# Performance work log

Measured on AMD Instinct MI355X. Metric: run time of the kernel, lower is better.

## Reference

```python
import jax, jax.numpy as jnp
import numpy as np

N_QUBITS = 8    # out_channels = number of wires
KERNEL = 4      # kernel_size
N_LAYERS = 3
PAD = 1
STRIDE = 1


def _gate_rx(t):
    c = jnp.cos(t / 2).astype(jnp.complex64)
    s = (-1j) * jnp.sin(t / 2).astype(jnp.complex64)
    return jnp.stack([jnp.stack([c, s]), jnp.stack([s, c])])


def _gate_ry(t):
    c = jnp.cos(t / 2).astype(jnp.complex64)
    s = jnp.sin(t / 2).astype(jnp.complex64)
    return jnp.stack([jnp.stack([c, -s]), jnp.stack([s, c])])


def _gate_rz(t):
    tc = t.astype(jnp.complex64)
    e0 = jnp.exp(-0.5j * tc)
    e1 = jnp.exp(0.5j * tc)
    z = jnp.zeros_like(e0)
    return jnp.stack([jnp.stack([e0, z]), jnp.stack([z, e1])])


def _apply1(state, gate, q):
    # state: (W, 2, ..., 2); shared 2x2 gate on qubit axis 1+q
    s = jnp.moveaxis(state, 1 + q, -1)
    s = jnp.einsum('...a,ba->...b', s, gate)
    return jnp.moveaxis(s, -1, 1 + q)


def _apply_ry_batched(state, theta, q):
    # per-window RY angles theta: (W,)
    c = jnp.cos(theta / 2)
    s = jnp.sin(theta / 2)
    g = jnp.stack([jnp.stack([c, -s], -1), jnp.stack([s, c], -1)], -2).astype(jnp.complex64)  # (W,2,2)
    st = jnp.moveaxis(state, 1 + q, -1)
    st = jnp.einsum('w...a,wba->w...b', st, g)
    return jnp.moveaxis(st, -1, 1 + q)


def _apply_cnot(state, c, t):
    # control qubit c, target qubit t (axes 1+c, 1+t)
    s = jnp.moveaxis(state, 1 + c, 1)
    ta = 2 + t if t < c else 1 + t
    s = jnp.moveaxis(s, ta, 2)
    s = jnp.stack([s[:, 0], jnp.flip(s[:, 1], axis=1)], axis=1)
    s = jnp.moveaxis(s, 2, ta)
    return jnp.moveaxis(s, 1, 1 + c)


def _ansatz(state, w):
    # custom_ansatz: per wire j: RX(w[j]); CNOT; RY(w[j]); CNOT; RZ(w[j]) with ring entanglement
    for j in range(N_QUBITS):
        cw, tw = (j, j + 1) if j < N_QUBITS - 1 else (0, N_QUBITS - 1)
        state = _apply1(state, _gate_rx(w[j]), j)
        state = _apply_cnot(state, cw, tw)
        state = _apply1(state, _gate_ry(w[j]), j)
        state = _apply_cnot(state, cw, tw)
        state = _apply1(state, _gate_rz(w[j]), j)
    return state

_ansatz_ckpt = jax.checkpoint(_ansatz)


@jax.jit
def _circuit(windows, weights):
    # windows: (W, KERNEL); weights: (N_LAYERS+1, N_QUBITS)
    W = windows.shape[0]
    state = jnp.zeros((W,) + (2,) * N_QUBITS, jnp.complex64)
    state = state.at[(slice(None),) + (0,) * N_QUBITS].set(1.0)
    state = _ansatz_ckpt(state, weights[0])
    for k in range(KERNEL):  # 'no_reupload' data encoding, once
        state = _apply_ry_batched(state, windows[:, k], k)
    for i in range(1, N_LAYERS + 1):
        state = _ansatz_ckpt(state, weights[i])
    probs = state.real ** 2 + state.imag ** 2
    evs = []
    for j in range(N_QUBITS):
        axes = tuple(a for a in range(1, N_QUBITS + 1) if a != 1 + j)
        p = probs.sum(axis=axes)  # (W, 2)
        evs.append(p[:, 0] - p[:, 1])
    return jnp.stack(evs, axis=-1)  # (W, N_QUBITS)


def setup_inputs() -> dict:
    key = jax.random.key(0)
    k1, k2 = jax.random.split(key)
    vector = jax.random.normal(k1, (32, 1, 512), jnp.float32)
    weights = jax.random.uniform(k2, (N_LAYERS + 1, N_QUBITS), jnp.float32, 0.0, 2.0 * np.pi)
    return {"vector": vector, "weights": weights}


def reference(vector, weights):
    bs, ch, l = vector.shape
    if ch > 1:
        vector = vector.mean(axis=1, keepdims=True)
    v = jnp.pad(vector[:, 0], ((0, 0), (PAD, PAD)))
    l_out = (l + 2 * PAD - KERNEL) // STRIDE + 1
    idx = jnp.arange(0, l_out, STRIDE)[:, None] + jnp.arange(KERNEL)[None, :]
    windows = v[:, idx].reshape(-1, KERNEL)  # (bs*l_out, KERNEL)
    out = _circuit(windows, weights)
    return out.reshape(bs, l_out, N_QUBITS).transpose(0, 2, 1).astype(jnp.float32)
```

## Files before the change

### kernel.cpp

```cpp
#include <hip/hip_runtime.h>
#include <math.h>


#define DEV __device__ __forceinline__

#define NQ 8
#define LOUT 511
#define LIN 512
#define BS 32
#define NPAIR 136

DEV float sx(float v, int m) { return __shfl_xor(v, m, 64); }

template<int J>
DEV void rot_rx(float (&re)[4], float (&im)[4], float c, float s) {
    if constexpr (J == 0) {
        float r0=re[0], i0=im[0], r2=re[2], i2=im[2];
        re[0]=c*r0+s*i2; im[0]=c*i0-s*r2; re[2]=c*r2+s*i0; im[2]=c*i2-s*r0;
        float r1=re[1], i1=im[1], r3=re[3], i3=im[3];
        re[1]=c*r1+s*i3; im[1]=c*i1-s*r3; re[3]=c*r3+s*i1; im[3]=c*i3-s*r1;
    } else if constexpr (J == 1) {
        float r0=re[0], i0=im[0], r1=re[1], i1=im[1];
        re[0]=c*r0+s*i1; im[0]=c*i0-s*r1; re[1]=c*r1+s*i0; im[1]=c*i1-s*r0;
        float r2=re[2], i2=im[2], r3=re[3], i3=im[3];
        re[2]=c*r2+s*i3; im[2]=c*i2-s*r3; re[3]=c*r3+s*i2; im[3]=c*i3-s*r2;
    } else {
        constexpr int m = 1 << (7 - J);
        #pragma unroll
        for (int r = 0; r < 4; ++r) {
            float pre = sx(re[r], m), pim = sx(im[r], m);
            re[r] = c*re[r] + s*pim;
            im[r] = c*im[r] - s*pre;
        }
    }
}

template<int J>
DEV void rot_ry(float (&re)[4], float (&im)[4], float c, float s, int lane) {
    if constexpr (J == 0) {
        float r0=re[0], i0=im[0], r2=re[2], i2=im[2];
        re[0]=c*r0-s*r2; im[0]=c*i0-s*i2; re[2]=s*r0+c*r2; im[2]=s*i0+c*i2;
        float r1=re[1], i1=im[1], r3=re[3], i3=im[3];
        re[1]=c*r1-s*r3; im[1]=c*i1-s*i3; re[3]=s*r1+c*r3; im[3]=s*i1+c*i3;
    } else if constexpr (J == 1) {
        float r0=re[0], i0=im[0], r1=re[1], i1=im[1];
        re[0]=c*r0-s*r1; im[0]=c*i0-s*i1; re[1]=s*r0+c*r1; im[1]=s*i0+c*i1;
        float r2=re[2], i2=im[2], r3=re[3], i3=im[3];
        re[2]=c*r2-s*r3; im[2]=c*i2-s*i3; re[3]=s*r2+c*r3; im[3]=s*i2+c*i3;
    } else {
        constexpr int m = 1 << (7 - J);
        float sg = (lane & m) ? s : -s;
        #pragma unroll
        for (int r = 0; r < 4; ++r) {
            float pre = sx(re[r], m), pim = sx(im[r], m);
            re[r] = c*re[r] + sg*pre;
            im[r] = c*im[r] + sg*pim;
        }
    }
}

template<int J>
DEV void rot_rz(float (&re)[4], float (&im)[4], float c, float s, int lane) {
    if constexpr (J == 0) {
        float t;
        t=re[0]; re[0]=c*t+s*im[0]; im[0]=c*im[0]-s*t;
        t=re[1]; re[1]=c*t+s*im[1]; im[1]=c*im[1]-s*t;
        t=re[2]; re[2]=c*t-s*im[2]; im[2]=c*im[2]+s*t;
        t=re[3]; re[3]=c*t-s*im[3]; im[3]=c*im[3]+s*t;
    } else if constexpr (J == 1) {
        float t;
        t=re[0]; re[0]=c*t+s*im[0]; im[0]=c*im[0]-s*t;
        t=re[2]; re[2]=c*t+s*im[2]; im[2]=c*im[2]-s*t;
        t=re[1]; re[1]=c*t-s*im[1]; im[1]=c*im[1]+s*t;
        t=re[3]; re[3]=c*t-s*im[3]; im[3]=c*im[3]+s*t;
    } else {
        constexpr int m = 1 << (7 - J);
        float sg = (lane & m) ? -s : s;
        #pragma unroll
        for (int r = 0; r < 4; ++r) {
            float t = re[r];
            re[r] = c*t + sg*im[r];
            im[r] = c*im[r] - sg*t;
        }
    }
}

template<int J>
DEV void cnot_w(float (&re)[4], float (&im)[4], int lane) {
    if constexpr (J == 0) {
        float t;
        t=re[2]; re[2]=re[3]; re[3]=t;
        t=im[2]; im[2]=im[3]; im[3]=t;
    } else if constexpr (J == 1) {
        re[1]=sx(re[1],32); im[1]=sx(im[1],32);
        re[3]=sx(re[3],32); im[3]=sx(im[3],32);
    } else if constexpr (J == 7) {
        re[2]=sx(re[2],1); im[2]=sx(im[2],1);
        re[3]=sx(re[3],1); im[3]=sx(im[3],1);
    } else {
        constexpr int mc = 1 << (7 - J);
        constexpr int mt = 1 << (6 - J);
        bool ctrl = (lane & mc) != 0;
        #pragma unroll
        for (int r = 0; r < 4; ++r) {
            float pre = sx(re[r], mt), pim = sx(im[r], mt);
            re[r] = ctrl ? pre : re[r];
            im[r] = ctrl ? pim : im[r];
        }
    }
}

template<int J>
DEV void wire(float (&re)[4], float (&im)[4], float ang, int lane) {
    float h = 0.5f * ang;
    float c = __cosf(h);
    float s = __sinf(h);
    rot_rx<J>(re, im, c, s);
    cnot_w<J>(re, im, lane);
    rot_ry<J>(re, im, c, s, lane);
    cnot_w<J>(re, im, lane);
    rot_rz<J>(re, im, c, s, lane);
}

DEV void ansatz(float (&re)[4], float (&im)[4], const float* __restrict__ w, int lane) {
    wire<0>(re, im, w[0], lane);
    wire<1>(re, im, w[1], lane);
    wire<2>(re, im, w[2], lane);
    wire<3>(re, im, w[3], lane);
    wire<4>(re, im, w[4], lane);
    wire<5>(re, im, w[5], lane);
    wire<6>(re, im, w[6], lane);
    wire<7>(re, im, w[7], lane);
}

__global__ __launch_bounds__(64) void kA1(const float* __restrict__ wts,
                                          float2* __restrict__ q) {
    int lane = threadIdx.x;
    int b = blockIdx.x;
    float re[4] = {0.f,0.f,0.f,0.f}, im[4] = {0.f,0.f,0.f,0.f};
    if (lane == 0) re[0] = 1.0f;
    ansatz(re, im, wts, lane);

    if (b & 1) {
        float t;
        t=re[0]; re[0]=-re[2]; re[2]=t;  t=im[0]; im[0]=-im[2]; im[2]=t;
        t=re[1]; re[1]=-re[3]; re[3]=t;  t=im[1]; im[1]=-im[3]; im[3]=t;
    }
    if (b & 2) {
        float t;
        t=re[0]; re[0]=-re[1]; re[1]=t;  t=im[0]; im[0]=-im[1]; im[1]=t;
        t=re[2]; re[2]=-re[3]; re[3]=t;  t=im[2]; im[2]=-im[3]; im[3]=t;
    }
    if (b & 4) {
        bool hi = (lane & 32) != 0;
        #pragma unroll
        for (int r = 0; r < 4; ++r) {
            float pre = sx(re[r],32), pim = sx(im[r],32);
            re[r] = hi ? pre : -pre;
            im[r] = hi ? pim : -pim;
        }
    }
    if (b & 8) {
        bool hi = (lane & 16) != 0;
        #pragma unroll
        for (int r = 0; r < 4; ++r) {
            float pre = sx(re[r],16), pim = sx(im[r],16);
            re[r] = hi ? pre : -pre;
            im[r] = hi ? pim : -pim;
        }
    }
    ansatz(re, im, wts + 8,  lane);
    ansatz(re, im, wts + 16, lane);
    ansatz(re, im, wts + 24, lane);
    #pragma unroll
    for (int r = 0; r < 4; ++r)
        q[b*256 + r*64 + lane] = make_float2(re[r], im[r]);
}

__global__ __launch_bounds__(64) void kA2(const float2* __restrict__ q,
                                          float* __restrict__ Sc) {
    int lane = threadIdx.x;
    int m = blockIdx.x;
    int b = 0, rem = m;
    while (rem >= 16 - b) { rem -= 16 - b; ++b; }
    int bp = b + rem;

    float pp[4];
    #pragma unroll
    for (int rr = 0; rr < 4; ++rr) {
        float2 x = q[b *256 + rr*64 + lane];
        float2 y = q[bp*256 + rr*64 + lane];
        pp[rr] = x.x*y.x + x.y*y.y;
    }
    float a0  = (pp[0]+pp[1]) - (pp[2]+pp[3]);
    float a1  = (pp[0]+pp[2]) - (pp[1]+pp[3]);
    float tot =  pp[0]+pp[1]+pp[2]+pp[3];

    #pragma unroll
    for (int mk = 1; mk <= 32; mk <<= 1) { a0 += sx(a0, mk); a1 += sx(a1, mk); }
    #pragma unroll
    for (int mk = 1; mk <= 32; mk <<= 1) {
        float p = sx(tot, mk);
        tot = (lane & mk) ? (p - tot) : (tot + p);
    }
    float scale = (b == bp) ? 1.0f : 2.0f;
    if (lane == 0) { Sc[m*8+0] = scale*a0; Sc[m*8+1] = scale*a1; }
    if (lane == 32) Sc[m*8+2] = scale*tot;
    if (lane == 16) Sc[m*8+3] = scale*tot;
    if (lane ==  8) Sc[m*8+4] = scale*tot;
    if (lane ==  4) Sc[m*8+5] = scale*tot;
    if (lane ==  2) Sc[m*8+6] = scale*tot;
    if (lane ==  1) Sc[m*8+7] = scale*tot;
}

__global__ __launch_bounds__(64) void kB(const float* __restrict__ vec,
                                         const float* __restrict__ Sc,
                                         float* __restrict__ out) {
    int lane = threadIdx.x;
    int o    = blockIdx.x * 64 + lane;
    int bat  = blockIdx.y;
    bool valid = o < LOUT;
    int oc = valid ? o : 0;

    float cs[4], sn[4];
    #pragma unroll
    for (int k = 0; k < 4; ++k) {
        int p = oc + k;
        float x = (p >= 1 && p <= LIN) ? vec[bat*LIN + p - 1] : 0.f;
        sn[k] = __sinf(0.5f*x);
        cs[k] = __cosf(0.5f*x);
    }
    float t[16];
    #pragma unroll
    for (int i = 0; i < 16; ++i)
        t[i] = ((i&1)?sn[0]:cs[0]) * ((i&2)?sn[1]:cs[1])
             * ((i&4)?sn[2]:cs[2]) * ((i&8)?sn[3]:cs[3]);

    float acc[8] = {0.f,0.f,0.f,0.f,0.f,0.f,0.f,0.f};
    int m = 0;
    #pragma unroll
    for (int b = 0; b < 16; ++b) {
        #pragma unroll
        for (int bp = b; bp < 16; ++bp) {
            float p = t[b] * t[bp];
            #pragma unroll
            for (int j = 0; j < 8; ++j)
                acc[j] = fmaf(Sc[m*8 + j], p, acc[j]);
            ++m;
        }
    }
    if (valid) {
        #pragma unroll
        for (int j = 0; j < 8; ++j)
            out[(bat*NQ + j)*LOUT + o] = acc[j];
    }
}

extern "C" void kernel_launch(void* const* d_in, const int* in_sizes, int n_in,
                              void* d_out, int out_size, void* d_ws, size_t ws_size,
                              hipStream_t stream) {
    const float* vec = (const float*)d_in[0];
    const float* wts = (const float*)d_in[1];
    float* out = (float*)d_out;
    float2* q  = (float2*)d_ws;
    float*  Sc = (float*)d_ws + 8192;
    kA1<<<16,  64, 0, stream>>>(wts, q);
    kA2<<<136, 64, 0, stream>>>(q, Sc);
    kB<<<dim3(8, BS), 64, 0, stream>>>(vec, Sc, out);
}
```

Measured before the change: 77.82 us.

## Fuse state-prep and pair-overlap kernels, recomputing both states per pair block

Merges the kernel that simulates the 16 basis-conditioned states with the kernel that computes the 136 pairwise overlaps. Each pair block now recomputes both states in registers and interleaves the two simulations, which removes one launch and the global write/read of the state buffer. In exchange every block repeats the circuit simulation, so total arithmetic grows roughly 17x, though it is spread across 136 blocks in parallel.

```diff
diff --git a/kernel.cpp b/kernel.cpp
--- a/kernel.cpp
+++ b/kernel.cpp
@@ -111,10 +111,7 @@
 }
 
 template<int J>
-DEV void wire(float (&re)[4], float (&im)[4], float ang, int lane) {
-    float h = 0.5f * ang;
-    float c = __cosf(h);
-    float s = __sinf(h);
+DEV void wire(float (&re)[4], float (&im)[4], float c, float s, int lane) {
     rot_rx<J>(re, im, c, s);
     cnot_w<J>(re, im, lane);
     rot_ry<J>(re, im, c, s, lane);
@@ -122,25 +119,30 @@
     rot_rz<J>(re, im, c, s, lane);
 }
 
-DEV void ansatz(float (&re)[4], float (&im)[4], const float* __restrict__ w, int lane) {
-    wire<0>(re, im, w[0], lane);
-    wire<1>(re, im, w[1], lane);
-    wire<2>(re, im, w[2], lane);
-    wire<3>(re, im, w[3], lane);
-    wire<4>(re, im, w[4], lane);
-    wire<5>(re, im, w[5], lane);
-    wire<6>(re, im, w[6], lane);
-    wire<7>(re, im, w[7], lane);
-}
-
-__global__ __launch_bounds__(64) void kA1(const float* __restrict__ wts,
-                                          float2* __restrict__ q) {
-    int lane = threadIdx.x;
-    int b = blockIdx.x;
-    float re[4] = {0.f,0.f,0.f,0.f}, im[4] = {0.f,0.f,0.f,0.f};
-    if (lane == 0) re[0] = 1.0f;
-    ansatz(re, im, wts, lane);
-
+DEV void ansatz1(float (&re)[4], float (&im)[4], const float* __restrict__ w, int lane) {
+    { float h=0.5f*w[0], c=__cosf(h), s=__sinf(h); wire<0>(re, im, c, s, lane); }
+    { float h=0.5f*w[1], c=__cosf(h), s=__sinf(h); wire<1>(re, im, c, s, lane); }
+    { float h=0.5f*w[2], c=__cosf(h), s=__sinf(h); wire<2>(re, im, c, s, lane); }
+    { float h=0.5f*w[3], c=__cosf(h), s=__sinf(h); wire<3>(re, im, c, s, lane); }
+    { float h=0.5f*w[4], c=__cosf(h), s=__sinf(h); wire<4>(re, im, c, s, lane); }
+    { float h=0.5f*w[5], c=__cosf(h), s=__sinf(h); wire<5>(re, im, c, s, lane); }
+    { float h=0.5f*w[6], c=__cosf(h), s=__sinf(h); wire<6>(re, im, c, s, lane); }
+    { float h=0.5f*w[7], c=__cosf(h), s=__sinf(h); wire<7>(re, im, c, s, lane); }
+}
+
+DEV void ansatz2(float (&xr)[4], float (&xi)[4], float (&yr)[4], float (&yi)[4],
+                 const float* __restrict__ w, int lane) {
+    { float h=0.5f*w[0], c=__cosf(h), s=__sinf(h); wire<0>(xr,xi,c,s,lane); wire<0>(yr,yi,c,s,lane); }
+    { float h=0.5f*w[1], c=__cosf(h), s=__sinf(h); wire<1>(xr,xi,c,s,lane); wire<1>(yr,yi,c,s,lane); }
+    { float h=0.5f*w[2], c=__cosf(h), s=__sinf(h); wire<2>(xr,xi,c,s,lane); wire<2>(yr,yi,c,s,lane); }
+    { float h=0.5f*w[3], c=__cosf(h), s=__sinf(h); wire<3>(xr,xi,c,s,lane); wire<3>(yr,yi,c,s,lane); }
+    { float h=0.5f*w[4], c=__cosf(h), s=__sinf(h); wire<4>(xr,xi,c,s,lane); wire<4>(yr,yi,c,s,lane); }
+    { float h=0.5f*w[5], c=__cosf(h), s=__sinf(h); wire<5>(xr,xi,c,s,lane); wire<5>(yr,yi,c,s,lane); }
+    { float h=0.5f*w[6], c=__cosf(h), s=__sinf(h); wire<6>(xr,xi,c,s,lane); wire<6>(yr,yi,c,s,lane); }
+    { float h=0.5f*w[7], c=__cosf(h), s=__sinf(h); wire<7>(xr,xi,c,s,lane); wire<7>(yr,yi,c,s,lane); }
+}
+
+DEV void applyG(float (&re)[4], float (&im)[4], int b, int lane) {
     if (b & 1) {
         float t;
         t=re[0]; re[0]=-re[2]; re[2]=t;  t=im[0]; im[0]=-im[2]; im[2]=t;
@@ -169,15 +171,9 @@
             im[r] = hi ? pim : -pim;
         }
     }
-    ansatz(re, im, wts + 8,  lane);
-    ansatz(re, im, wts + 16, lane);
-    ansatz(re, im, wts + 24, lane);
-    #pragma unroll
-    for (int r = 0; r < 4; ++r)
-        q[b*256 + r*64 + lane] = make_float2(re[r], im[r]);
-}
-
-__global__ __launch_bounds__(64) void kA2(const float2* __restrict__ q,
+}
+
+__global__ __launch_bounds__(64) void kAB(const float* __restrict__ wts,
                                           float* __restrict__ Sc) {
     int lane = threadIdx.x;
     int m = blockIdx.x;
@@ -185,13 +181,25 @@
     while (rem >= 16 - b) { rem -= 16 - b; ++b; }
     int bp = b + rem;
 
+    float xr[4] = {0.f,0.f,0.f,0.f}, xi[4] = {0.f,0.f,0.f,0.f};
+    if (lane == 0) xr[0] = 1.0f;
+    ansatz1(xr, xi, wts, lane);
+
+    float yr[4], yi[4];
+    #pragma unroll
+    for (int r = 0; r < 4; ++r) { yr[r] = xr[r]; yi[r] = xi[r]; }
+    applyG(xr, xi, b,  lane);
+    applyG(yr, yi, bp, lane);
+
+    ansatz2(xr, xi, yr, yi, wts + 8,  lane);
+    ansatz2(xr, xi, yr, yi, wts + 16, lane);
+    ansatz2(xr, xi, yr, yi, wts + 24, lane);
+
     float pp[4];
     #pragma unroll
-    for (int rr = 0; rr < 4; ++rr) {
-        float2 x = q[b *256 + rr*64 + lane];
-        float2 y = q[bp*256 + rr*64 + lane];
-        pp[rr] = x.x*y.x + x.y*y.y;
-    }
+    for (int r = 0; r < 4; ++r)
+        pp[r] = xr[r]*yr[r] + xi[r]*yi[r];
+
     float a0  = (pp[0]+pp[1]) - (pp[2]+pp[3]);
     float a1  = (pp[0]+pp[2]) - (pp[1]+pp[3]);
     float tot =  pp[0]+pp[1]+pp[2]+pp[3];
@@ -262,9 +270,7 @@
     const float* vec = (const float*)d_in[0];
     const float* wts = (const float*)d_in[1];
     float* out = (float*)d_out;
-    float2* q  = (float2*)d_ws;
-    float*  Sc = (float*)d_ws + 8192;
-    kA1<<<16,  64, 0, stream>>>(wts, q);
-    kA2<<<136, 64, 0, stream>>>(q, Sc);
+    float* Sc  = (float*)d_ws;
+    kAB<<<NPAIR, 64, 0, stream>>>(wts, Sc);
     kB<<<dim3(8, BS), 64, 0, stream>>>(vec, Sc, out);
 }
```

Measured after the change: 84.04 us. 8.0% more time.
